# Kernel optimization log

Hardware: AMD Instinct MI355X
Metric: run time of the kernel (lower is better)

## Reference

```python
import jax, jax.numpy as jnp
import numpy as np

NINPUTS = 16
WIDTH = 128
KSIZE = 21
SPP = 8
BS, CI, H, W = 2, 3, 192, 192
EPS = 1e-08


def _conv(x, w, b, padding):
    y = jax.lax.conv_general_dilated(
        x, w, window_strides=(1, 1), padding=padding,
        dimension_numbers=("NCHW", "OIHW", "NCHW"))
    return y + b[None, :, None, None]


def apply_kernels(kernel, radiance, ksize):
    """Per-pixel predicted-kernel conv: fused gather-multiply-reduce over taps.
    kernel: (bs, ksize^2, kh, kw), radiance: (bs, ci, h, w).
    Replicates torch apply_kernels (normalization='sum') without materializing
    the (bs, ci, kh, kw, ksize^2) unfold tile tensor."""
    bs, k2, kh, kw = kernel.shape
    _, ci, h, w = radiance.shape
    needed = kh + ksize - 1
    if needed > h:
        crop = (needed - h) // 2
        if crop > 0:
            kernel = kernel[:, :, crop:-crop, crop:-crop]
        kh, kw = kernel.shape[2], kernel.shape[3]
    else:
        crop = (h - needed) // 2
        if crop > 0:
            radiance = radiance[:, :, crop:-crop, crop:-crop]
    taps = jnp.arange(k2, dtype=jnp.int32)
    dy = taps // ksize
    dx = taps % ksize

    def body(acc, idx):
        patch = jax.lax.dynamic_slice(radiance, (0, 0, dy[idx], dx[idx]),
                                      (bs, ci, kh, kw))
        kv = jax.lax.dynamic_slice_in_dim(kernel, idx, 1, axis=1)  # (bs,1,kh,kw)
        return acc + kv * patch, None

    acc0 = jnp.zeros((bs, ci, kh, kw), radiance.dtype)
    weighted_sum, _ = jax.lax.scan(body, acc0, taps)
    kernel_sum = jnp.sum(kernel, axis=1, keepdims=True)  # (bs,1,kh,kw)
    return weighted_sum, kernel_sum


def setup_inputs() -> dict:
    key = jax.random.key(0)
    ks = jax.random.split(key, 10)
    s = 0.05
    inp = {
        "features": jax.random.normal(ks[0], (BS, SPP, NINPUTS, H, W), jnp.float32),
        "radiance": jax.random.uniform(ks[1], (BS, SPP, CI, H, W), jnp.float32),
        # recurrent conv processor (simplified main_processor): SAME 3x3 conv
        "w_rnn": jax.random.normal(ks[2], (WIDTH, NINPUTS + WIDTH, 3, 3), jnp.float32) * s,
        "b_rnn": jnp.zeros((WIDTH,), jnp.float32),
        "w_k1": jax.random.normal(ks[3], (WIDTH, WIDTH + NINPUTS, 3, 3), jnp.float32) * s,
        "b_k1": jnp.zeros((WIDTH,), jnp.float32),
        "w_k2": jax.random.normal(ks[4], (WIDTH, WIDTH, 3, 3), jnp.float32) * s,
        "b_k2": jnp.zeros((WIDTH,), jnp.float32),
        "w_k3": jax.random.normal(ks[5], (KSIZE * KSIZE, WIDTH, 3, 3), jnp.float32) * s,
        "b_k3": jnp.zeros((KSIZE * KSIZE,), jnp.float32),
    }
    return inp


def reference(features, radiance, w_rnn, b_rnn, w_k1, b_k1, w_k2, b_k2, w_k3, b_k3):
    bs, spp, ci, h, w = radiance.shape
    lrelu = lambda x: jax.nn.leaky_relu(x, 0.01)
    state = jnp.zeros((bs, WIDTH, h, w), features.dtype)
    unnorm = sumw = max_k = None
    for step in range(spp):
        f = features[:, step]  # (bs, ninputs, h, w)
        rnn = lrelu(_conv(jnp.concatenate([f, state], axis=1), w_rnn, b_rnn, "SAME"))
        state = rnn
        nf = jnp.concatenate([rnn, f], axis=1)  # (bs, width+ninputs, h, w)
        k = lrelu(_conv(nf, w_k1, b_k1, "VALID"))
        k = lrelu(_conv(k, w_k2, b_k2, "VALID"))
        k = _conv(k, w_k3, b_k3, "VALID")  # (bs, ksize^2, h-6, w-6), linear out
        # online-softmax (flash-attention-style) running max/exp rescale
        new_max = jnp.max(k.reshape(bs, -1), axis=1).reshape(bs, 1, 1, 1)
        if step == 0:
            max_k = new_max
        else:
            old_max = max_k
            max_k = jnp.maximum(old_max, new_max)
        kern = jnp.exp(k - max_k)
        ws, ksum = apply_kernels(kern, radiance[:, step], KSIZE)
        if step == 0:
            unnorm, sumw = ws, ksum
        else:
            scale = jnp.exp(old_max - max_k)
            unnorm = unnorm * scale + ws
            sumw = sumw * scale + ksum
    return unnorm / (sumw + EPS)
```

## Files before the change

### kernel.cpp

```cpp
#include <hip/hip_runtime.h>
#include <stdint.h>

typedef _Float16 half8 __attribute__((ext_vector_type(8)));
typedef _Float16 half4 __attribute__((ext_vector_type(4)));
typedef __attribute__((ext_vector_type(8))) short short8;
typedef __attribute__((ext_vector_type(4))) float f32x4;
typedef __attribute__((ext_vector_type(16))) float f32x16;

__device__ __forceinline__ unsigned encf(float x){
  uint32_t u = __float_as_uint(x);
  return (u & 0x80000000u) ? ~u : (u | 0x80000000u);
}
__device__ __forceinline__ float decf(unsigned u){
  uint32_t b = (u & 0x80000000u) ? (u & 0x7FFFFFFFu) : ~u;
  return __uint_as_float(b);
}
__device__ __forceinline__ void gload16(const void* g, void* l){
  __builtin_amdgcn_global_load_lds(
      (const __attribute__((address_space(1))) void*)g,
      (__attribute__((address_space(3))) void*)l, 16, 0, 0);
}

__global__ __launch_bounds__(256) void zero_u32(unsigned* __restrict__ p, int n){
  for (int i = blockIdx.x*256 + threadIdx.x; i < n; i += gridDim.x*256) p[i] = 0u;
}

__global__ __launch_bounds__(256) void pack_w(const float* __restrict__ w, _Float16* __restrict__ wp,
                                              int CO, int CI, int COP, int CINP){
  int idx = blockIdx.x*256 + threadIdx.x;
  int total = 9*COP*CINP;
  if (idx >= total) return;
  int ci = idx % CINP;
  int rest = idx / CINP;
  int co = rest % COP;
  int t  = rest / COP;
  float v = 0.f;
  if (co < CO && ci < CI) v = w[((size_t)co*CI + ci)*9 + t];
  int kc = ci >> 4, chl = ci & 15;
  wp[(((size_t)kc*9 + t)*(COP/32) + (co>>5))*512 + (co&31)*16 + chl] = (_Float16)v;
}

__global__ __launch_bounds__(256) void pack_bias(const float* __restrict__ b, float* __restrict__ bp, int n, int npad){
  int i = blockIdx.x*256 + threadIdx.x;
  if (i < npad) bp[i] = (i < n) ? b[i] : 0.f;
}

__global__ __launch_bounds__(256) void pack_feat(const float* __restrict__ f,
                                                 _Float16* __restrict__ rnn_in,
                                                 _Float16* __restrict__ k1_in,
                                                 int copy_state,
                                                 unsigned fbstr, unsigned rbstr, unsigned kbstr){
  int p = blockIdx.x*256 + threadIdx.x;
  if (p >= 36864) return;
  int b = blockIdx.y;
  int y = p / 192, x = p % 192;
  const float* fb = f + (size_t)b*fbstr;
  _Float16* r = rnn_in + (size_t)b*rbstr + ((size_t)(y+1)*194 + (x+1))*160;
  _Float16* k = k1_in  + (size_t)b*kbstr + (size_t)p*160;
  #pragma unroll
  for (int c = 0; c < 16; ++c){
    _Float16 v = (_Float16)fb[c*36864 + p];
    r[c] = v;
    k[128 + c] = v;
  }
  if (copy_state){
    #pragma unroll
    for (int cc = 0; cc < 128; cc += 8)
      *reinterpret_cast<short8*>(r + 16 + cc) = *reinterpret_cast<const short8*>(k + cc);
  }
}

template<int CINP, bool RELU, bool K3>
__global__ __launch_bounds__(128, 2) void conv3(
    const _Float16* __restrict__ X, int Wst, unsigned xbstr,
    const _Float16* __restrict__ Wp, int COP,
    const float* __restrict__ bias,
    _Float16* __restrict__ Y, int Wst_out, int DCP, unsigned ybstr,
    unsigned* __restrict__ slot, int Ho, int Wo,
    int nco)
{
  constexpr int KC    = CINP/16;
  constexpr int SROWS = K3 ? 10 : 6;
  constexpr int ITEMS = SROWS*34*2;
  constexpr int NRND  = (ITEMS + 127)/128;
  __shared__ _Float16 lds[2][ITEMS*8];

  const int tid  = threadIdx.x;
  const int lane = tid & 63;
  const int wid  = tid >> 6;
  const int l31  = lane & 31;
  const int hsel = lane >> 5;
  const int xb   = blockIdx.x * 32;
  const int yb   = blockIdx.y * (K3 ? 8 : 4);
  const int co_blk = blockIdx.z % nco;
  const int b      = blockIdx.z / nco;

  const _Float16* Xb = X + (size_t)b * xbstr;
  const int NG = COP/32;
  const size_t wtap = (size_t)NG*512;
  const _Float16* wbase = Wp
      + ((size_t)(K3 ? (co_blk*2) : (co_blk*4 + wid*2)))*512 + l31*16 + hsel*8;

  uint32_t goff[NRND];
  #pragma unroll
  for (int k = 0; k < NRND; ++k){
    int item = k*128 + tid;
    if (item < ITEMS){
      int row  = item / 68;
      int rem  = item % 68;
      int col  = rem >> 1;
      int half = rem & 1;
      int pix  = (yb + row)*Wst + xb + col;
      goff[k] = (uint32_t)(((uint32_t)pix*CINP + half*8) * 2);
    } else goff[k] = 0;
  }

  auto stage = [&](int buf, int kc){
    const char* xp = (const char*)Xb + (size_t)kc*32;
    char* lb = (char*)&lds[buf][0];
    #pragma unroll
    for (int k = 0; k < NRND; ++k){
      if (k*128 + tid < ITEMS)
        gload16(xp + goff[k], lb + k*2048 + wid*1024);
    }
  };

  uint32_t boffe[4];
  #pragma unroll
  for (int n = 0; n < 4; ++n){
    const int row = K3 ? (wid*4 + n) : n;
    boffe[n] = (uint32_t)((row*34 + l31)*16 + hsel*8);
  }

  f32x16 acc[4][2] = {};
  half8 wreg[3][2];
  #pragma unroll
  for (int s3 = 0; s3 < 3; ++s3)
    #pragma unroll
    for (int g = 0; g < 2; ++g)
      wreg[s3][g] = *reinterpret_cast<const half8*>(wbase + (size_t)s3*wtap + g*512);

  stage(0, 0);
  __syncthreads();
  for (int kc = 0; kc < KC; ++kc){
    if (kc + 1 < KC) stage((kc+1)&1, kc+1);
    const _Float16* wt = wbase + (size_t)(kc*9)*wtap;
    const _Float16* lb = &lds[kc&1][0];
    half8 breg[2][4];
    #pragma unroll
    for (int n = 0; n < 4; ++n)
      breg[0][n] = *reinterpret_cast<const half8*>(lb + boffe[n]);
    #pragma unroll
    for (int t = 0; t < 9; ++t){
      const int cur = t & 1, nxt = cur ^ 1;
      if (t < 8){
        const int ky1 = (t+1)/3, kx1 = (t+1) - ky1*3;
        #pragma unroll
        for (int n = 0; n < 4; ++n)
          breg[nxt][n] = *reinterpret_cast<const half8*>(lb + boffe[n] + (ky1*34 + kx1)*16);
      }
      #pragma unroll
      for (int n = 0; n < 4; ++n)
        #pragma unroll
        for (int g = 0; g < 2; ++g)
          acc[n][g] = __builtin_amdgcn_mfma_f32_32x32x16_f16(
              wreg[t % 3][g], breg[cur][n], acc[n][g], 0, 0, 0);
      #pragma unroll
      for (int g = 0; g < 2; ++g)
        wreg[t % 3][g] = *reinterpret_cast<const half8*>(wt + (size_t)(t+3)*wtap + g*512);
    }
    if (kc + 1 < KC) __syncthreads();
  }

  const int x = xb + l31;
  float lmax = -3.0e38f;
  #pragma unroll
  for (int n = 0; n < 4; ++n){
    const int y = yb + (K3 ? (wid*4 + n) : n);
    if (y < Ho && x < Wo){
      #pragma unroll
      for (int g = 0; g < 2; ++g){
        #pragma unroll
        for (int q = 0; q < 4; ++q){
          const int cb = (K3 ? (co_blk*64 + g*32) : (co_blk*128 + (wid*2 + g)*32))
                         + 4*hsel + 8*q;
          f32x4 bs = *reinterpret_cast<const f32x4*>(bias + cb);
          float v[4];
          #pragma unroll
          for (int j = 0; j < 4; ++j){
            float tv = acc[n][g][q*4 + j] + bs[j];
            if (RELU) tv = tv > 0.f ? tv : 0.01f*tv;
            v[j] = tv;
          }
          if constexpr (!K3){
            half4 pk;
            #pragma unroll
            for (int j = 0; j < 4; ++j) pk[j] = (_Float16)v[j];
            *reinterpret_cast<half4*>(Y + (size_t)b*ybstr + ((size_t)y*Wst_out + x)*DCP + cb) = pk;
          } else {
            _Float16* yp = Y + (size_t)b*ybstr;
            #pragma unroll
            for (int j = 0; j < 4; ++j){
              if (cb + j < 441){
                yp[(size_t)(cb+j)*29584 + (size_t)y*172 + x] = (_Float16)v[j];
                lmax = fmaxf(lmax, v[j]);
              }
            }
          }
        }
      }
    }
  }
  if constexpr (K3){
    #pragma unroll
    for (int o = 32; o > 0; o >>= 1) lmax = fmaxf(lmax, __shfl_xor(lmax, o));
    if (lane == 0) atomicMax(slot + b, encf(lmax));
  }
}

__global__ void update_max(float* __restrict__ st, unsigned* __restrict__ slot, int step){
  int b = threadIdx.x;
  if (b < 2){
    float nm   = decf(slot[b]);
    float oldM = st[2*b];
    float M    = (step == 0) ? nm : fmaxf(oldM, nm);
    st[2*b+1] = (step == 0) ? 0.f : expf(oldM - M);
    st[2*b]   = M;
    slot[b] = 0u;
  }
}

__global__ __launch_bounds__(256) void apply_acc(
    const _Float16* __restrict__ k3out, const float* __restrict__ rad,
    const float* __restrict__ st,
    float* __restrict__ unnorm, float* __restrict__ sumw)
{
  const int tx = threadIdx.x & 63, ty = threadIdx.x >> 6;
  const int x = blockIdx.x*64 + tx;
  const int y = blockIdx.y*4 + ty;
  const int b = blockIdx.z;
  if (x >= 172 || y >= 172) return;
  const float M = st[2*b], scale = st[2*b+1];
  const _Float16* kp = k3out + (size_t)b*13046544 + (size_t)y*172 + x;
  const float* rb = rad + (size_t)b*884736;
  float a0 = 0.f, a1 = 0.f, a2 = 0.f, aw = 0.f;
  for (int dy = 0; dy < 21; ++dy){
    const float* r0 = rb + (size_t)(y+dy)*192 + x;
    #pragma unroll
    for (int dx = 0; dx < 21; ++dx){
      float w = __expf((float)kp[(size_t)(dy*21+dx)*29584] - M);
      aw += w;
      a0 += w * r0[dx];
      a1 += w * r0[36864 + dx];
      a2 += w * r0[73728 + dx];
    }
  }
  size_t p = (size_t)b*88752 + (size_t)y*172 + x;
  size_t ps = (size_t)b*29584 + (size_t)y*172 + x;
  unnorm[p]        = unnorm[p]*scale        + a0;
  unnorm[p+29584]  = unnorm[p+29584]*scale  + a1;
  unnorm[p+59168]  = unnorm[p+59168]*scale  + a2;
  sumw[ps]         = sumw[ps]*scale         + aw;
}

__global__ __launch_bounds__(256) void finalize_out(const float* __restrict__ unnorm,
                                                    const float* __restrict__ sumw,
                                                    float* __restrict__ out){
  int i = blockIdx.x*256 + threadIdx.x;
  int b = blockIdx.y;
  if (i >= 88752) return;
  int p = i % 29584;
  out[(size_t)b*88752 + i] = unnorm[(size_t)b*88752 + i] / (sumw[(size_t)b*29584 + p] + 1e-8f);
}

extern "C" void kernel_launch(void* const* d_in, const int* in_sizes, int n_in,
                              void* d_out, int out_size, void* d_ws, size_t ws_size,
                              hipStream_t stream) {
  const float* features = (const float*)d_in[0];
  const float* radiance = (const float*)d_in[1];
  const float* w_rnn = (const float*)d_in[2];
  const float* b_rnn = (const float*)d_in[3];
  const float* w_k1  = (const float*)d_in[4];
  const float* b_k1  = (const float*)d_in[5];
  const float* w_k2  = (const float*)d_in[6];
  const float* b_k2  = (const float*)d_in[7];
  const float* w_k3  = (const float*)d_in[8];
  const float* b_k3  = (const float*)d_in[9];
  float* out = (float*)d_out;

  char* ws = (char*)d_ws;
  size_t off = 0;
  auto alloc = [&](size_t bytes)->char*{
    char* p = ws + off;
    off = (off + bytes + 255) & ~(size_t)255;
    return p;
  };
  const size_t WSLACK = 98304;
  _Float16* wp_rnn   = (_Float16*)alloc((size_t)9*128*160*2 + WSLACK);
  _Float16* wp_k1    = (_Float16*)alloc((size_t)9*128*160*2 + WSLACK);
  _Float16* wp_k2    = (_Float16*)alloc((size_t)9*128*128*2 + WSLACK);
  _Float16* wp_k3    = (_Float16*)alloc((size_t)9*448*128*2 + WSLACK);
  float*    bias_k3p = (float*)   alloc((size_t)448*4);
  const unsigned RB  = 194u*194u*160u;
  const unsigned KB  = (194u*192u+64u)*160u;
  const unsigned K2B = (194u*190u+64u)*128u;
  const unsigned K3B = (194u*188u+64u)*128u;
  const unsigned KOB = 441u*29584u;
  _Float16* rnn_in = (_Float16*)alloc((size_t)2*RB*2);
  _Float16* k1_in  = (_Float16*)alloc((size_t)2*KB*2);
  _Float16* k2_in  = (_Float16*)alloc((size_t)2*K2B*2);
  _Float16* k3_in  = (_Float16*)alloc((size_t)2*K3B*2);
  _Float16* k3_out = (_Float16*)alloc((size_t)2*KOB*2);
  float*    accz   = (float*)   alloc((size_t)236678*4);
  if (off > ws_size) return;

  float*    unnorm = accz;
  float*    sumw   = accz + 177504;
  float*    st     = accz + 236672;
  unsigned* slot   = (unsigned*)(accz + 236676);

  pack_w<<<(9*128*160+255)/256, 256, 0, stream>>>(w_rnn, wp_rnn, 128, 144, 128, 160);
  pack_w<<<(9*128*160+255)/256, 256, 0, stream>>>(w_k1,  wp_k1,  128, 144, 128, 160);
  pack_w<<<(9*128*128+255)/256, 256, 0, stream>>>(w_k2,  wp_k2,  128, 128, 128, 128);
  pack_w<<<(9*448*128+255)/256, 256, 0, stream>>>(w_k3,  wp_k3,  441, 128, 448, 128);
  pack_bias<<<2, 256, 0, stream>>>(b_k3, bias_k3p, 441, 448);

  zero_u32<<<2048, 256, 0, stream>>>((unsigned*)rnn_in, (int)(2*RB/2));
  zero_u32<<<925,  256, 0, stream>>>((unsigned*)accz, 236678);

  for (int s = 0; s < 8; ++s){
    const float* f   = features + (size_t)s*16*36864;
    const float* rad = radiance + (size_t)s*3*36864;
    pack_feat<<<dim3(144,2), 256, 0, stream>>>(f, rnn_in, k1_in, s > 0 ? 1 : 0,
                                               8u*16u*36864u, RB, KB);
    conv3<160,true ,false><<<dim3(6,48,2), 128, 0, stream>>>(
        rnn_in, 194, RB, wp_rnn, 128, b_rnn, k1_in, 192, 160, KB,
        nullptr, 192, 192, 1);
    conv3<160,true ,false><<<dim3(6,48,2), 128, 0, stream>>>(
        k1_in, 192, KB, wp_k1, 128, b_k1, k2_in, 190, 128, K2B,
        nullptr, 190, 190, 1);
    conv3<128,true ,false><<<dim3(6,47,2), 128, 0, stream>>>(
        k2_in, 190, K2B, wp_k2, 128, b_k2, k3_in, 188, 128, K3B,
        nullptr, 188, 188, 1);
    conv3<128,false,true ><<<dim3(6,22,14), 128, 0, stream>>>(
        k3_in + (size_t)(7*188 + 7)*128, 188, K3B, wp_k3, 448, bias_k3p,
        k3_out, 0, 0, KOB, slot, 172, 172, 7);
    update_max<<<1, 64, 0, stream>>>(st, slot, s);
    apply_acc<<<dim3(3,43,2), 256, 0, stream>>>(k3_out, rad, st, unnorm, sumw);
  }
  finalize_out<<<dim3(347,2), 256, 0, stream>>>(unnorm, sumw, out);
}
```

Measured before the change: 2.357 ms.

## Trim channel padding, double-buffer RNN state, and crop k1/k2 convs to needed region

Input channel padding for the rnn and k1 convolutions drops from 160 to 144, cutting MMA work and memory traffic by a tenth. The rnn conv now also writes its output straight into a ping-ponged padded rnn input buffer, so pack_feat no longer copies the state. The k1 and k2 convolutions now compute only the cropped region that the k3 conv and kernel application actually consume (178 and 174 instead of 190 and 188), skipping border work. The risk is that the crop offsets and strides must line up exactly with the k3 input window, and the 144-channel tiling must still work with the KC loop in the conv kernel.

```diff
diff --git a/kernel.cpp b/kernel.cpp
--- a/kernel.cpp
+++ b/kernel.cpp
@@ -46,36 +46,31 @@
 }
 
 __global__ __launch_bounds__(256) void pack_feat(const float* __restrict__ f,
-                                                 _Float16* __restrict__ rnn_in,
+                                                 _Float16* __restrict__ rnn_b,
                                                  _Float16* __restrict__ k1_in,
-                                                 int copy_state,
                                                  unsigned fbstr, unsigned rbstr, unsigned kbstr){
   int p = blockIdx.x*256 + threadIdx.x;
   if (p >= 36864) return;
   int b = blockIdx.y;
   int y = p / 192, x = p % 192;
   const float* fb = f + (size_t)b*fbstr;
-  _Float16* r = rnn_in + (size_t)b*rbstr + ((size_t)(y+1)*194 + (x+1))*160;
-  _Float16* k = k1_in  + (size_t)b*kbstr + (size_t)p*160;
+  _Float16* r = rnn_b + (size_t)b*rbstr + ((size_t)(y+1)*194 + (x+1))*144;
+  _Float16* k = k1_in + (size_t)b*kbstr + (size_t)p*144;
   #pragma unroll
   for (int c = 0; c < 16; ++c){
     _Float16 v = (_Float16)fb[c*36864 + p];
     r[c] = v;
     k[128 + c] = v;
   }
-  if (copy_state){
-    #pragma unroll
-    for (int cc = 0; cc < 128; cc += 8)
-      *reinterpret_cast<short8*>(r + 16 + cc) = *reinterpret_cast<const short8*>(k + cc);
-  }
-}
-
-template<int CINP, bool RELU, bool K3>
+}
+
+template<int CINP, bool RELU, bool K3, bool DUAL>
 __global__ __launch_bounds__(128, 2) void conv3(
     const _Float16* __restrict__ X, int Wst, unsigned xbstr,
     const _Float16* __restrict__ Wp, int COP,
     const float* __restrict__ bias,
     _Float16* __restrict__ Y, int Wst_out, int DCP, unsigned ybstr,
+    _Float16* __restrict__ Y2, unsigned y2str,
     unsigned* __restrict__ slot, int Ho, int Wo,
     int nco)
 {
@@ -182,7 +177,7 @@
       for (int g = 0; g < 2; ++g){
         #pragma unroll
         for (int q = 0; q < 4; ++q){
-          const int cb = (K3 ? (co_blk*64 + g*32) : (co_blk*128 + (wid*2 + g)*32))
+          const int cb = (K3 ? (co_blk*64 + g*32) : ((wid*2 + g)*32))
                          + 4*hsel + 8*q;
           f32x4 bs = *reinterpret_cast<const f32x4*>(bias + cb);
           float v[4];
@@ -197,6 +192,9 @@
             #pragma unroll
             for (int j = 0; j < 4; ++j) pk[j] = (_Float16)v[j];
             *reinterpret_cast<half4*>(Y + (size_t)b*ybstr + ((size_t)y*Wst_out + x)*DCP + cb) = pk;
+            if constexpr (DUAL)
+              *reinterpret_cast<half4*>(Y2 + (size_t)b*y2str
+                  + ((size_t)(y+1)*194 + (x+1))*144 + 16 + cb) = pk;
           } else {
             _Float16* yp = Y + (size_t)b*ybstr;
             #pragma unroll
@@ -296,17 +294,18 @@
     return p;
   };
   const size_t WSLACK = 98304;
-  _Float16* wp_rnn   = (_Float16*)alloc((size_t)9*128*160*2 + WSLACK);
-  _Float16* wp_k1    = (_Float16*)alloc((size_t)9*128*160*2 + WSLACK);
+  _Float16* wp_rnn   = (_Float16*)alloc((size_t)9*128*144*2 + WSLACK);
+  _Float16* wp_k1    = (_Float16*)alloc((size_t)9*128*144*2 + WSLACK);
   _Float16* wp_k2    = (_Float16*)alloc((size_t)9*128*128*2 + WSLACK);
   _Float16* wp_k3    = (_Float16*)alloc((size_t)9*448*128*2 + WSLACK);
   float*    bias_k3p = (float*)   alloc((size_t)448*4);
-  const unsigned RB  = 194u*194u*160u;
-  const unsigned KB  = (194u*192u+64u)*160u;
+  const unsigned RB  = 194u*194u*144u;
+  const unsigned KB  = (192u*192u+64u)*144u;
   const unsigned K2B = (194u*190u+64u)*128u;
   const unsigned K3B = (194u*188u+64u)*128u;
   const unsigned KOB = 441u*29584u;
-  _Float16* rnn_in = (_Float16*)alloc((size_t)2*RB*2);
+  _Float16* rnn_inA = (_Float16*)alloc((size_t)2*RB*2);
+  _Float16* rnn_inB = (_Float16*)alloc((size_t)2*RB*2);
   _Float16* k1_in  = (_Float16*)alloc((size_t)2*KB*2);
   _Float16* k2_in  = (_Float16*)alloc((size_t)2*K2B*2);
   _Float16* k3_in  = (_Float16*)alloc((size_t)2*K3B*2);
@@ -319,32 +318,39 @@
   float*    st     = accz + 236672;
   unsigned* slot   = (unsigned*)(accz + 236676);
 
-  pack_w<<<(9*128*160+255)/256, 256, 0, stream>>>(w_rnn, wp_rnn, 128, 144, 128, 160);
-  pack_w<<<(9*128*160+255)/256, 256, 0, stream>>>(w_k1,  wp_k1,  128, 144, 128, 160);
+  _Float16* rnn_buf[2] = { rnn_inA, rnn_inB };
+
+  pack_w<<<(9*128*144+255)/256, 256, 0, stream>>>(w_rnn, wp_rnn, 128, 144, 128, 144);
+  pack_w<<<(9*128*144+255)/256, 256, 0, stream>>>(w_k1,  wp_k1,  128, 144, 128, 144);
   pack_w<<<(9*128*128+255)/256, 256, 0, stream>>>(w_k2,  wp_k2,  128, 128, 128, 128);
   pack_w<<<(9*448*128+255)/256, 256, 0, stream>>>(w_k3,  wp_k3,  441, 128, 448, 128);
   pack_bias<<<2, 256, 0, stream>>>(b_k3, bias_k3p, 441, 448);
 
-  zero_u32<<<2048, 256, 0, stream>>>((unsigned*)rnn_in, (int)(2*RB/2));
+  zero_u32<<<2048, 256, 0, stream>>>((unsigned*)rnn_inA, (int)RB);
+  zero_u32<<<2048, 256, 0, stream>>>((unsigned*)rnn_inB, (int)RB);
   zero_u32<<<925,  256, 0, stream>>>((unsigned*)accz, 236678);
 
   for (int s = 0; s < 8; ++s){
     const float* f   = features + (size_t)s*16*36864;
     const float* rad = radiance + (size_t)s*3*36864;
-    pack_feat<<<dim3(144,2), 256, 0, stream>>>(f, rnn_in, k1_in, s > 0 ? 1 : 0,
+    _Float16* rcur = rnn_buf[s & 1];
+    _Float16* rnxt = rnn_buf[(s + 1) & 1];
+    pack_feat<<<dim3(144,2), 256, 0, stream>>>(f, rcur, k1_in,
                                                8u*16u*36864u, RB, KB);
-    conv3<160,true ,false><<<dim3(6,48,2), 128, 0, stream>>>(
-        rnn_in, 194, RB, wp_rnn, 128, b_rnn, k1_in, 192, 160, KB,
-        nullptr, 192, 192, 1);
-    conv3<160,true ,false><<<dim3(6,48,2), 128, 0, stream>>>(
-        k1_in, 192, KB, wp_k1, 128, b_k1, k2_in, 190, 128, K2B,
-        nullptr, 190, 190, 1);
-    conv3<128,true ,false><<<dim3(6,47,2), 128, 0, stream>>>(
-        k2_in, 190, K2B, wp_k2, 128, b_k2, k3_in, 188, 128, K3B,
-        nullptr, 188, 188, 1);
-    conv3<128,false,true ><<<dim3(6,22,14), 128, 0, stream>>>(
+    conv3<144,true ,false,true ><<<dim3(6,48,2), 128, 0, stream>>>(
+        rcur, 194, RB, wp_rnn, 128, b_rnn, k1_in, 192, 144, KB,
+        rnxt, RB, nullptr, 192, 192, 1);
+    conv3<144,true ,false,false><<<dim3(6,45,2), 128, 0, stream>>>(
+        k1_in + (size_t)(7*192 + 7)*144, 192, KB, wp_k1, 128, b_k1,
+        k2_in + (size_t)(7*190 + 7)*128, 190, 128, K2B,
+        nullptr, 0, nullptr, 178, 178, 1);
+    conv3<128,true ,false,false><<<dim3(6,44,2), 128, 0, stream>>>(
+        k2_in + (size_t)(7*190 + 7)*128, 190, K2B, wp_k2, 128, b_k2,
+        k3_in + (size_t)(7*188 + 7)*128, 188, 128, K3B,
+        nullptr, 0, nullptr, 174, 174, 1);
+    conv3<128,false,true ,false><<<dim3(6,22,14), 128, 0, stream>>>(
         k3_in + (size_t)(7*188 + 7)*128, 188, K3B, wp_k3, 448, bias_k3p,
-        k3_out, 0, 0, KOB, slot, 172, 172, 7);
+        k3_out, 0, 0, KOB, nullptr, 0, slot, 172, 172, 7);
     update_max<<<1, 64, 0, stream>>>(st, slot, s);
     apply_acc<<<dim3(3,43,2), 256, 0, stream>>>(k3_out, rad, st, unnorm, sumw);
   }
```

Result: faster. 2.265 ms (-3.9%).
